# Kernel tuning notes

Hardware: AMD Instinct MI355X
Metric: run time of the kernel (lower is better)

## Reference

```python
import jax, jax.numpy as jnp
import numpy as np
import math

EMBED_DIM = 96
NUM_HEADS = 4
HEAD_DIM = EMBED_DIM // NUM_HEADS
RANGE_SIZES = (7, 9, 11)
SCALE = math.sqrt(HEAD_DIM)


def setup_inputs() -> dict:
    key = jax.random.key(0)
    ks = jax.random.split(key, 10)
    B, C, H, W = 2, EMBED_DIM, 64, 64
    s = 1.0 / math.sqrt(C)
    x = jax.random.normal(ks[0], (B, C, H, W), dtype=jnp.float32)
    wq = jax.random.normal(ks[1], (C, C), dtype=jnp.float32) * s
    bq = jax.random.normal(ks[2], (C,), dtype=jnp.float32) * 0.01
    wk = jax.random.normal(ks[3], (C, C), dtype=jnp.float32) * s
    bk = jax.random.normal(ks[4], (C,), dtype=jnp.float32) * 0.01
    wv = jax.random.normal(ks[5], (C, C), dtype=jnp.float32) * s
    bv = jax.random.normal(ks[6], (C,), dtype=jnp.float32) * 0.01
    wo = jax.random.normal(ks[7], (C, C * len(RANGE_SIZES)), dtype=jnp.float32) * (1.0 / math.sqrt(C * len(RANGE_SIZES)))
    bo = jax.random.normal(ks[8], (C,), dtype=jnp.float32) * 0.01
    return {"x": x, "wq": wq, "bq": bq, "wk": wk, "bk": bk,
            "wv": wv, "bv": bv, "wo": wo, "bo": bo}


def _conv1x1(x, w, b):
    # x: (B,Cin,H,W), w: (Cout,Cin) -> (B,Cout,H,W)
    return jnp.einsum('oc,bchw->bohw', w, x) + b[None, :, None, None]


def _unfold_patches(t, k):
    # t: (B,n,d,H,W) -> (B,n,d,k*k,H*W), zero-padded local neighborhoods,
    # kernel offsets row-major to match torch F.unfold ordering.
    B, n, d, H, W = t.shape
    p = k // 2
    tp = jnp.pad(t, ((0, 0), (0, 0), (0, 0), (p, p), (p, p)))
    pats = jnp.stack([tp[..., i:i + H, j:j + W]
                      for i in range(k) for j in range(k)], axis=3)
    return pats.reshape(B, n, d, k * k, H * W)


def reference(x, wq, bq, wk, bk, wv, bv, wo, bo):
    B, C, H, W = x.shape
    n, d = NUM_HEADS, HEAD_DIM
    Q = _conv1x1(x, wq, bq).reshape(B, n, d, H, W)
    K = _conv1x1(x, wk, bk).reshape(B, n, d, H, W)
    V = _conv1x1(x, wv, bv).reshape(B, n, d, H, W)
    Q_flat = Q.reshape(B, n, d, H * W)
    outputs = []
    for k in RANGE_SIZES:
        Kp = _unfold_patches(K, k)  # (B,n,d,kk,HW)
        Vp = _unfold_patches(V, k)
        scores = jnp.einsum('bndh,bndrh->bnrh', Q_flat, Kp) / SCALE
        attn = jax.nn.softmax(scores, axis=2)
        outputs.append(jnp.einsum('bnrh,bndrh->bndh', attn, Vp))
    concat = jnp.concatenate(outputs, axis=2)  # (B,n,d*len(ranges),HW)
    concat = concat.reshape(B, n * d * len(RANGE_SIZES), H, W)
    return _conv1x1(concat, wo, bo)
```

## Files before the change

### kernel.cpp

```cpp
#include <hip/hip_runtime.h>
#include <hip/hip_fp16.h>


#define HW    4096
#define NH    4
#define D     24
#define CC    96
#define C3    288
#define BATCH 2

#define TS    8
#define HALO  5
#define SW    18
#define SPIX  324
#define PSTR  24

#define INV_SCALE 0.20412414523193151f

typedef unsigned short u16;
typedef _Float16 h2f __attribute__((ext_vector_type(2)));

__device__ __forceinline__ float fdot2h(unsigned int a, unsigned int b, float c) {
#if __has_builtin(__builtin_amdgcn_fdot2)
    return __builtin_amdgcn_fdot2(__builtin_bit_cast(h2f, a),
                                  __builtin_bit_cast(h2f, b), c, false);
#else
    float2 fa = __half22float2(__builtin_bit_cast(__half2, a));
    float2 fb = __half22float2(__builtin_bit_cast(__half2, b));
    return fmaf(fa.x, fb.x, fmaf(fa.y, fb.y, c));
#endif
}

__device__ __forceinline__ unsigned int packh2(float a, float b) {
    return __builtin_bit_cast(unsigned int, __floats2half2_rn(a, b));
}

__global__ void prep_w(const float* __restrict__ wo, unsigned int* __restrict__ wh) {
    int idx = blockIdx.x * 256 + threadIdx.x;
    if (idx < CC * (C3 / 2)) {
        int o  = idx / (C3 / 2);
        int c2 = idx - o * (C3 / 2);
        wh[idx] = packh2(wo[o * C3 + 2 * c2], wo[o * C3 + 2 * c2 + 1]);
    }
}

__global__ __launch_bounds__(256) void qkv_kernel(
    const float* __restrict__ x,
    const float* __restrict__ wq, const float* __restrict__ bq,
    const float* __restrict__ wk, const float* __restrict__ bk,
    const float* __restrict__ wv, const float* __restrict__ bv,
    u16* __restrict__ Qh, u16* __restrict__ Kh, u16* __restrict__ Vh)
{
    __shared__ __align__(16) float xs[CC * 64];

    int t   = threadIdx.x;
    int mat = blockIdx.y;
    const float* w    = (mat == 0) ? wq : (mat == 1) ? wk : wv;
    const float* bias = (mat == 0) ? bq : (mat == 1) ? bk : bv;
    u16* dst          = (mat == 0) ? Qh : (mat == 1) ? Kh : Vh;

    int gp0 = blockIdx.x * 64;
    int b   = gp0 >> 12;
    int p0  = gp0 & 4095;

    const float4* xsrc = (const float4*)(x + (size_t)b * CC * HW + p0);
    #pragma unroll
    for (int k = 0; k < 6; ++k) {
        int u   = t + k * 256;
        int c   = u >> 4;
        int px4 = u & 15;
        float4 v = xsrc[(size_t)c * (HW / 4) + px4];
        *(float4*)&xs[c * 64 + px4 * 4] = v;
    }
    __syncthreads();

    int wvid = __builtin_amdgcn_readfirstlane(t >> 6);
    int o0   = blockIdx.z * 48 + wvid * 12;
    int px   = t & 63;
    int gp   = gp0 + px;

    float acc[12];
    #pragma unroll
    for (int j = 0; j < 12; ++j) acc[j] = bias[o0 + j];

    #pragma unroll
    for (int cb = 0; cb < 3; ++cb) {
        float xc[32];
        #pragma unroll
        for (int i = 0; i < 32; ++i) xc[i] = xs[(cb * 32 + i) * 64 + px];
        #pragma unroll
        for (int j = 0; j < 12; ++j) {
            const float* wr = w + (o0 + j) * CC + cb * 32;
            #pragma unroll
            for (int i = 0; i < 32; ++i) acc[j] = fmaf(wr[i], xc[i], acc[j]);
        }
    }

    unsigned int u[6];
    #pragma unroll
    for (int i = 0; i < 6; ++i) u[i] = packh2(acc[2 * i], acc[2 * i + 1]);
    uint2* dp = (uint2*)(dst + (size_t)gp * CC + o0);
    dp[0] = make_uint2(u[0], u[1]);
    dp[1] = make_uint2(u[2], u[3]);
    dp[2] = make_uint2(u[4], u[5]);
}

__global__ __launch_bounds__(256) void attn_kernel(
    const u16* __restrict__ Qh, const u16* __restrict__ Kh,
    const u16* __restrict__ Vh, u16* __restrict__ att)
{
    __shared__ __align__(16) u16 smem[2 * SPIX * PSTR];
    u16* Ks = smem;
    u16* Vs = smem + SPIX * PSTR;
    float* Pb = (float*)smem;

    int t    = threadIdx.x;
    int wvid = t >> 6, lane = t & 63;
    int bh = blockIdx.z;
    int b  = bh >> 2, h = bh & 3;
    int x0 = blockIdx.x * TS, y0 = blockIdx.y * TS;

    for (int sp = t; sp < SPIX; sp += 256) {
        int sy = sp / SW, sx = sp - sy * SW;
        int gy = y0 + sy - HALO, gx = x0 + sx - HALO;
        uint4 k0 = make_uint4(0,0,0,0), k1 = k0, k2 = k0;
        uint4 v0 = k0, v1 = k0, v2 = k0;
        if ((unsigned)gy < 64u && (unsigned)gx < 64u) {
            size_t base = ((size_t)(b * HW + gy * 64 + gx) * CC + h * D);
            const uint4* ksrc = (const uint4*)(Kh + base);
            const uint4* vsrc = (const uint4*)(Vh + base);
            k0 = ksrc[0]; k1 = ksrc[1]; k2 = ksrc[2];
            v0 = vsrc[0]; v1 = vsrc[1]; v2 = vsrc[2];
        }
        uint4* kd = (uint4*)(Ks + sp * PSTR);
        uint4* vd = (uint4*)(Vs + sp * PSTR);
        kd[0] = k0; kd[1] = k1; kd[2] = k2;
        vd[0] = v0; vd[1] = v1; vd[2] = v2;
    }
    __syncthreads();

    int ty = lane >> 3, tx = lane & 7;
    int gp = b * HW + (y0 + ty) * 64 + (x0 + tx);

    unsigned int q[12];
    {
        const uint4* qs = (const uint4*)(Qh + (size_t)gp * CC + h * D);
        uint4 a = qs[0], bb = qs[1], c = qs[2];
        q[0]=a.x;  q[1]=a.y;  q[2]=a.z;  q[3]=a.w;
        q[4]=bb.x; q[5]=bb.y; q[6]=bb.z; q[7]=bb.w;
        q[8]=c.x;  q[9]=c.y;  q[10]=c.z; q[11]=c.w;
    }

    float acc[D];
    #pragma unroll
    for (int j = 0; j < D; ++j) acc[j] = 0.f;
    float l  = 0.f;
    int   cp = (ty + HALO) * SW + (tx + HALO);

    auto visit = [&](int di, int dj) {
        int sp = cp + di * SW + dj;
        const uint4* kp = (const uint4*)(Ks + sp * PSTR);
        uint4 k0 = kp[0], k1 = kp[1], k2 = kp[2];
        unsigned int ku[12] = {k0.x,k0.y,k0.z,k0.w, k1.x,k1.y,k1.z,k1.w, k2.x,k2.y,k2.z,k2.w};
        float s = 0.f;
        #pragma unroll
        for (int i = 0; i < 12; ++i) s = fdot2h(ku[i], q[i], s);
        float pw = __expf(s * INV_SCALE);
        l += pw;
        const uint4* vp = (const uint4*)(Vs + sp * PSTR);
        uint4 v0 = vp[0], v1 = vp[1], v2 = vp[2];
        unsigned int vu[12] = {v0.x,v0.y,v0.z,v0.w, v1.x,v1.y,v1.z,v1.w, v2.x,v2.y,v2.z,v2.w};
        #pragma unroll
        for (int i = 0; i < 12; ++i) {
            float2 f = __half22float2(__builtin_bit_cast(__half2, vu[i]));
            acc[2*i]   = fmaf(pw, f.x, acc[2*i]);
            acc[2*i+1] = fmaf(pw, f.y, acc[2*i+1]);
        }
    };

    if (wvid == 0) {
        #pragma unroll
        for (int k = 0; k < 49; k += 2) visit(k / 7 - 3, k % 7 - 3);
    } else if (wvid == 1) {
        #pragma unroll
        for (int k = 1; k < 49; k += 2) visit(k / 7 - 3, k % 7 - 3);
    } else if (wvid == 2) {
        #pragma unroll
        for (int dj = -4; dj <= 4; ++dj) { visit(-4, dj); visit(4, dj); }
        #pragma unroll
        for (int di = -3; di <= 3; ++di) { visit(di, -4); visit(di, 4); }
    } else {
        #pragma unroll
        for (int dj = -5; dj <= 5; ++dj) { visit(-5, dj); visit(5, dj); }
        #pragma unroll
        for (int di = -4; di <= 4; ++di) { visit(di, -5); visit(di, 5); }
    }

    __syncthreads();
    {
        float* pp = Pb + (wvid * 64 + lane) * 26;
        pp[0] = l;
        #pragma unroll
        for (int i = 0; i < D; ++i) pp[1 + i] = acc[i];
    }
    __syncthreads();

    if (wvid < 3) {
        float L = 0.f;
        float a[D];
        #pragma unroll
        for (int i = 0; i < D; ++i) a[i] = 0.f;
        #pragma unroll
        for (int s = 0; s < 4; ++s) {
            if (s <= wvid + 1) {
                const float* pp = Pb + (s * 64 + lane) * 26;
                L += pp[0];
                #pragma unroll
                for (int i = 0; i < D; ++i) a[i] += pp[1 + i];
            }
        }
        float rl = 1.0f / L;
        unsigned int u[12];
        #pragma unroll
        for (int i = 0; i < 12; ++i)
            u[i] = packh2(a[2 * i] * rl, a[2 * i + 1] * rl);
        uint4* dp = (uint4*)(att + (size_t)gp * C3 + h * 72 + wvid * D);
        dp[0] = make_uint4(u[0], u[1], u[2],  u[3]);
        dp[1] = make_uint4(u[4], u[5], u[6],  u[7]);
        dp[2] = make_uint4(u[8], u[9], u[10], u[11]);
    }
}

#define K3_PAD 65
__global__ __launch_bounds__(256) void proj_kernel(
    const u16* __restrict__ att, const unsigned int* __restrict__ wh,
    const float* __restrict__ bo, float* __restrict__ out)
{
    __shared__ unsigned int ab[(C3 / 2) * K3_PAD];

    int t   = threadIdx.x;
    int gp0 = blockIdx.x * 64;

    const uint4* src = (const uint4*)(att + (size_t)gp0 * C3);
    #pragma unroll
    for (int k = 0; k < 9; ++k) {
        int u   = t + k * 256;
        uint4 v = src[u];
        int px  = u / 36;
        int c20 = (u - px * 36) * 4;
        ab[(c20    ) * K3_PAD + px] = v.x;
        ab[(c20 + 1) * K3_PAD + px] = v.y;
        ab[(c20 + 2) * K3_PAD + px] = v.z;
        ab[(c20 + 3) * K3_PAD + px] = v.w;
    }
    __syncthreads();

    int wvid = __builtin_amdgcn_readfirstlane(t >> 6);
    int o0   = blockIdx.y * 24 + wvid * 6;
    int px   = t & 63;
    int gp   = gp0 + px;
    int b    = gp >> 12, p = gp & 4095;

    float acc[6];
    #pragma unroll
    for (int j = 0; j < 6; ++j) acc[j] = bo[o0 + j];

    #pragma unroll
    for (int cb = 0; cb < 9; ++cb) {
        unsigned int xp[16];
        #pragma unroll
        for (int i = 0; i < 16; ++i) xp[i] = ab[(cb * 16 + i) * K3_PAD + px];
        #pragma unroll
        for (int j = 0; j < 6; ++j) {
            const unsigned int* wr = wh + (o0 + j) * (C3 / 2) + cb * 16;
            #pragma unroll
            for (int i = 0; i < 16; ++i) acc[j] = fdot2h(xp[i], wr[i], acc[j]);
        }
    }

    #pragma unroll
    for (int j = 0; j < 6; ++j)
        out[(size_t)(b * CC + o0 + j) * HW + p] = acc[j];
}

extern "C" void kernel_launch(void* const* d_in, const int* in_sizes, int n_in,
                              void* d_out, int out_size, void* d_ws, size_t ws_size,
                              hipStream_t stream)
{
    const float* x  = (const float*)d_in[0];
    const float* wq = (const float*)d_in[1];
    const float* bq = (const float*)d_in[2];
    const float* wk = (const float*)d_in[3];
    const float* bk = (const float*)d_in[4];
    const float* wv = (const float*)d_in[5];
    const float* bv = (const float*)d_in[6];
    const float* wo = (const float*)d_in[7];
    const float* bo = (const float*)d_in[8];
    float* out = (float*)d_out;

    const size_t NPIX = (size_t)BATCH * HW;
    char* ws = (char*)d_ws;
    u16* Qh  = (u16*)ws;
    u16* Kh  = Qh + NPIX * CC;
    u16* Vh  = Kh + NPIX * CC;
    u16* att = Vh + NPIX * CC;
    unsigned int* wh = (unsigned int*)(att + NPIX * C3);

    prep_w<<<dim3(54), 256, 0, stream>>>(wo, wh);

    qkv_kernel<<<dim3(128, 3, 2), 256, 0, stream>>>(x, wq, bq, wk, bk, wv, bv, Qh, Kh, Vh);

    attn_kernel<<<dim3(8, 8, 8), 256, 0, stream>>>(Qh, Kh, Vh, att);

    proj_kernel<<<dim3(128, 4), 256, 0, stream>>>(att, wh, bo, out);
}
```

Measured before the change: 126.1 us.

## Split attention neighborhood across eight waves and read x directly in QKV

The attention kernel now launches 512 threads per tile, and each of eight waves takes a quarter of the 7x7 offsets or one half of a 9x9 or 11x11 ring. The per-wave partial sums are combined through a larger shared buffer with a padded stride. The change aims to shorten each wave's serial chain of neighbor visits and raise occupancy, at the cost of more shared-memory traffic in the reduction. Separately, the QKV projection drops its shared-memory staging of x and loads x from global memory per pixel in 16-channel chunks, removing a barrier but relying on the cache for reuse across waves.

Measured after the change: 127.7 us. No clear change (+1.2%).

```diff
diff --git a/kernel.cpp b/kernel.cpp
--- a/kernel.cpp
+++ b/kernel.cpp
@@ -14,6 +14,7 @@
 #define SW    18
 #define SPIX  324
 #define PSTR  24
+#define PBS   29
 
 #define INV_SCALE 0.20412414523193151f
 
@@ -51,48 +52,34 @@
     const float* __restrict__ wv, const float* __restrict__ bv,
     u16* __restrict__ Qh, u16* __restrict__ Kh, u16* __restrict__ Vh)
 {
-    __shared__ __align__(16) float xs[CC * 64];
-
     int t   = threadIdx.x;
     int mat = blockIdx.y;
     const float* w    = (mat == 0) ? wq : (mat == 1) ? wk : wv;
     const float* bias = (mat == 0) ? bq : (mat == 1) ? bk : bv;
     u16* dst          = (mat == 0) ? Qh : (mat == 1) ? Kh : Vh;
 
-    int gp0 = blockIdx.x * 64;
-    int b   = gp0 >> 12;
-    int p0  = gp0 & 4095;
-
-    const float4* xsrc = (const float4*)(x + (size_t)b * CC * HW + p0);
-    #pragma unroll
-    for (int k = 0; k < 6; ++k) {
-        int u   = t + k * 256;
-        int c   = u >> 4;
-        int px4 = u & 15;
-        float4 v = xsrc[(size_t)c * (HW / 4) + px4];
-        *(float4*)&xs[c * 64 + px4 * 4] = v;
-    }
-    __syncthreads();
-
-    int wvid = __builtin_amdgcn_readfirstlane(t >> 6);
-    int o0   = blockIdx.z * 48 + wvid * 12;
-    int px   = t & 63;
-    int gp   = gp0 + px;
+    int gp = blockIdx.x * 64 + (t & 63);
+    int b  = gp >> 12;
+    int p  = gp & 4095;
+    int o0 = blockIdx.z * 48 + __builtin_amdgcn_readfirstlane(t >> 6) * 12;
+
+    const float* xb = x + (size_t)b * CC * HW + p;
 
     float acc[12];
     #pragma unroll
     for (int j = 0; j < 12; ++j) acc[j] = bias[o0 + j];
 
     #pragma unroll
-    for (int cb = 0; cb < 3; ++cb) {
-        float xc[32];
-        #pragma unroll
-        for (int i = 0; i < 32; ++i) xc[i] = xs[(cb * 32 + i) * 64 + px];
+    for (int cb = 0; cb < 6; ++cb) {
+        float xc[16];
+        #pragma unroll
+        for (int i = 0; i < 16; ++i)
+            xc[i] = xb[(size_t)(cb * 16 + i) * HW];
         #pragma unroll
         for (int j = 0; j < 12; ++j) {
-            const float* wr = w + (o0 + j) * CC + cb * 32;
+            const float* wr = w + (o0 + j) * CC + cb * 16;
             #pragma unroll
-            for (int i = 0; i < 32; ++i) acc[j] = fmaf(wr[i], xc[i], acc[j]);
+            for (int i = 0; i < 16; ++i) acc[j] = fmaf(wr[i], xc[i], acc[j]);
         }
     }
 
@@ -105,22 +92,24 @@
     dp[2] = make_uint2(u[4], u[5]);
 }
 
-__global__ __launch_bounds__(256) void attn_kernel(
+__global__ __launch_bounds__(512) void attn_kernel(
     const u16* __restrict__ Qh, const u16* __restrict__ Kh,
     const u16* __restrict__ Vh, u16* __restrict__ att)
 {
-    __shared__ __align__(16) u16 smem[2 * SPIX * PSTR];
-    u16* Ks = smem;
-    u16* Vs = smem + SPIX * PSTR;
-    float* Pb = (float*)smem;
+    __shared__ __align__(16) char smem_raw[8 * 64 * PBS * 4];
+    u16* Ks = (u16*)smem_raw;
+    u16* Vs = Ks + SPIX * PSTR;
+    float* Pb = (float*)smem_raw;
 
     int t    = threadIdx.x;
-    int wvid = t >> 6, lane = t & 63;
+    int wvid = __builtin_amdgcn_readfirstlane(t >> 6);
+    int lane = t & 63;
     int bh = blockIdx.z;
     int b  = bh >> 2, h = bh & 3;
     int x0 = blockIdx.x * TS, y0 = blockIdx.y * TS;
 
-    for (int sp = t; sp < SPIX; sp += 256) {
+    if (t < SPIX) {
+        int sp = t;
         int sy = sp / SW, sx = sp - sy * SW;
         int gy = y0 + sy - HALO, gx = x0 + sx - HALO;
         uint4 k0 = make_uint4(0,0,0,0), k1 = k0, k2 = k0;
@@ -180,25 +169,41 @@
 
     if (wvid == 0) {
         #pragma unroll
-        for (int k = 0; k < 49; k += 2) visit(k / 7 - 3, k % 7 - 3);
+        for (int k = 0; k < 49; k += 4) visit(k / 7 - 3, k % 7 - 3);
     } else if (wvid == 1) {
         #pragma unroll
-        for (int k = 1; k < 49; k += 2) visit(k / 7 - 3, k % 7 - 3);
+        for (int k = 1; k < 49; k += 4) visit(k / 7 - 3, k % 7 - 3);
     } else if (wvid == 2) {
         #pragma unroll
-        for (int dj = -4; dj <= 4; ++dj) { visit(-4, dj); visit(4, dj); }
-        #pragma unroll
-        for (int di = -3; di <= 3; ++di) { visit(di, -4); visit(di, 4); }
+        for (int k = 2; k < 49; k += 4) visit(k / 7 - 3, k % 7 - 3);
+    } else if (wvid == 3) {
+        #pragma unroll
+        for (int k = 3; k < 49; k += 4) visit(k / 7 - 3, k % 7 - 3);
+    } else if (wvid == 4) {
+        #pragma unroll
+        for (int dj = -4; dj <= 4; ++dj) visit(-4, dj);
+        #pragma unroll
+        for (int di = -3; di <= 3; ++di) visit(di, -4);
+    } else if (wvid == 5) {
+        #pragma unroll
+        for (int dj = -4; dj <= 4; ++dj) visit(4, dj);
+        #pragma unroll
+        for (int di = -3; di <= 3; ++di) visit(di, 4);
+    } else if (wvid == 6) {
+        #pragma unroll
+        for (int dj = -5; dj <= 5; ++dj) visit(-5, dj);
+        #pragma unroll
+        for (int di = -4; di <= 4; ++di) visit(di, -5);
     } else {
         #pragma unroll
-        for (int dj = -5; dj <= 5; ++dj) { visit(-5, dj); visit(5, dj); }
-        #pragma unroll
-        for (int di = -4; di <= 4; ++di) { visit(di, -5); visit(di, 5); }
+        for (int dj = -5; dj <= 5; ++dj) visit(5, dj);
+        #pragma unroll
+        for (int di = -4; di <= 4; ++di) visit(di, 5);
     }
 
     __syncthreads();
     {
-        float* pp = Pb + (wvid * 64 + lane) * 26;
+        float* pp = Pb + (wvid * 64 + lane) * PBS;
         pp[0] = l;
         #pragma unroll
         for (int i = 0; i < D; ++i) pp[1 + i] = acc[i];
@@ -206,18 +211,16 @@
     __syncthreads();
 
     if (wvid < 3) {
+        int N = (wvid == 0) ? 4 : (wvid == 1) ? 6 : 8;
         float L = 0.f;
         float a[D];
         #pragma unroll
         for (int i = 0; i < D; ++i) a[i] = 0.f;
-        #pragma unroll
-        for (int s = 0; s < 4; ++s) {
-            if (s <= wvid + 1) {
-                const float* pp = Pb + (s * 64 + lane) * 26;
-                L += pp[0];
-                #pragma unroll
-                for (int i = 0; i < D; ++i) a[i] += pp[1 + i];
-            }
+        for (int s = 0; s < N; ++s) {
+            const float* pp = Pb + (s * 64 + lane) * PBS;
+            L += pp[0];
+            #pragma unroll
+            for (int i = 0; i < D; ++i) a[i] += pp[1 + i];
         }
         float rl = 1.0f / L;
         unsigned int u[12];
@@ -310,7 +313,7 @@
 
     qkv_kernel<<<dim3(128, 3, 2), 256, 0, stream>>>(x, wq, bq, wk, bk, wv, bv, Qh, Kh, Vh);
 
-    attn_kernel<<<dim3(8, 8, 8), 256, 0, stream>>>(Qh, Kh, Vh, att);
+    attn_kernel<<<dim3(8, 8, 8), 512, 0, stream>>>(Qh, Kh, Vh, att);
 
     proj_kernel<<<dim3(128, 4), 256, 0, stream>>>(att, wh, bo, out);
 }
```
